# Optimization experiments

Measured on AMD Instinct MI355X. Metric: run time of the kernel, lower is better.

Reference implementation:

```python
import jax, jax.numpy as jnp
import numpy as np

N_POWER_SERIES = 8  # 'fixed' estimator, n_power_series=8, n_samples=4 (leading axis of v)


def _g_fn(x, W1, b1, W2, b2):
    # residual branch g(x): Linear -> ELU -> Linear (canonical i-ResNet block)
    return jax.nn.elu(x @ W1 + b1) @ W2 + b2


def setup_inputs() -> dict:
    key = jax.random.key(0)
    ks = jax.random.split(key, 4)
    B, D, H, S = 8192, 1024, 4096, 4
    x = jax.random.normal(ks[0], (B, D), jnp.float32)
    # scale weights so g is roughly contractive (Lipschitz < 1), as spectral norm enforces
    W1 = jax.random.normal(ks[1], (D, H), jnp.float32) * (0.5 / np.sqrt(D))
    b1 = jnp.zeros((H,), jnp.float32)
    W2 = jax.random.normal(ks[2], (H, D), jnp.float32) * (0.5 / np.sqrt(H))
    b2 = jnp.zeros((D,), jnp.float32)
    v = jax.random.normal(ks[3], (S, B, D), jnp.float32)  # Hutchinson probes
    log_df_dz = jnp.zeros((B,), jnp.float32)
    return {"x": x, "log_df_dz": log_df_dz, "W1": W1, "b1": b1, "W2": W2, "b2": b2, "v": v}


def reference(x, log_df_dz, W1, b1, W2, b2, v):
    g, vjp_fn = jax.vjp(lambda xx: _g_fn(xx, W1, b1, W2, b2), x)
    vjp = lambda w: vjp_fn(w)[0]  # w^T J, w: [B, D]

    w = v                      # [S, B, D]
    sum_diag = jnp.zeros(v.shape[:2], v.dtype)  # [S, B]
    for k in range(1, N_POWER_SERIES + 1):
        w = jax.vmap(vjp)(w)                        # v^T J^k
        inner = jnp.einsum('sbd,sbd->sb', w, v)     # Hutchinson tr(J^k) estimate
        sign = 1.0 if (k % 2 == 1) else -1.0
        sum_diag = sum_diag + sign * (inner / k)
    logdet = jnp.mean(sum_diag, axis=0)             # mean over samples -> [B]

    z = x + g
    return z, log_df_dz + logdet
```

## Files before the change

### kernel.cpp

```cpp
#include <hip/hip_runtime.h>
#include <hip/hip_bf16.h>

using bf16 = __hip_bfloat16;
typedef __attribute__((ext_vector_type(8))) short bf16x8;
typedef __attribute__((ext_vector_type(4))) float f32x4;

__device__ __forceinline__ float b2f(unsigned short u) {
  union { unsigned int i; float f; } x; x.i = ((unsigned int)u) << 16; return x.f;
}
__device__ __forceinline__ unsigned short f2b(float f) {
  __hip_bfloat16 h = __float2bfloat16(f);
  return *reinterpret_cast<unsigned short*>(&h);
}

__device__ __forceinline__ void load16_to_lds(const bf16* g, void* lds) {
  __builtin_amdgcn_global_load_lds((const __attribute__((address_space(1))) void*)g,
                                   (__attribute__((address_space(3))) void*)lds, 16, 0, 0);
}

#define FENCE() asm volatile("" ::: "memory")
#define BAR() do { FENCE(); __builtin_amdgcn_s_barrier(); FENCE(); } while (0)
#define SCHED_PIN() __builtin_amdgcn_sched_barrier(0)

__global__ void cast_f32_bf16(const float* __restrict__ in, bf16* __restrict__ out, size_t n) {
  size_t i0 = ((size_t)blockIdx.x * 256 + threadIdx.x) * 4;
  size_t stride = (size_t)gridDim.x * 256 * 4;
  for (size_t i = i0; i < n; i += stride) {
    float4 f = *(const float4*)(in + i);
    ushort4 o;
    o.x = f2b(f.x); o.y = f2b(f.y); o.z = f2b(f.z); o.w = f2b(f.w);
    *(ushort4*)(out + i) = o;
  }
}

__global__ void transpose_cast(const float* __restrict__ in, bf16* __restrict__ out, int R, int C) {
  __shared__ float tile[32][33];
  int tx = threadIdx.x & 31, ty = threadIdx.x >> 5;
  int r0 = blockIdx.y * 32, c0 = blockIdx.x * 32;
  #pragma unroll
  for (int i = 0; i < 32; i += 8)
    tile[ty + i][tx] = in[(size_t)(r0 + ty + i) * C + (c0 + tx)];
  __syncthreads();
  #pragma unroll
  for (int i = 0; i < 32; i += 8)
    out[(size_t)(c0 + ty + i) * R + (r0 + tx)] = __float2bfloat16(tile[tx][ty + i]);
}

template<int EPI>
__global__ __launch_bounds__(512, 2)
void gemm256(const bf16* __restrict__ A, const bf16* __restrict__ Bm,
             int M, int N, int K,
             bf16* __restrict__ OutB,
             const float* __restrict__ bias,
             const bf16* __restrict__ Ea) {
  __shared__ __align__(16) char pool[131072];
  char* Albs = pool;
  char* Blbs = pool + 65536;
  const int tid = threadIdx.x;
  const int l = tid & 63, w = tid >> 6;
  const int lane16 = l & 15, lh = l >> 4;
  const int wr = w >> 2, wc = w & 3;
  const int bm0 = blockIdx.y * 256, bn0 = blockIdx.x * 256;
  const int NT2 = K >> 7;

  auto stage = [&](const bf16* G, int grow0, int kbase, char* ldsbase) {
    #pragma unroll
    for (int r = 0; r < 2; ++r) {
      int p = (r * 512 + tid) * 16;
      int row = p >> 7, colb = p & 127;
      int cs = colb ^ ((row & 7) << 4);
      const bf16* g = G + (size_t)(grow0 + row) * K + kbase + (cs >> 1);
      load16_to_lds(g, ldsbase + (size_t)(r * 512 + w * 64) * 16);
    }
  };
  auto rd = [&](const char* base, int row, int colb) -> bf16x8 {
    return *(const bf16x8*)(base + row * 128 + (colb ^ ((row & 7) << 4)));
  };

  f32x4 acc[8][4] = {};
  bf16x8 a_r[4][2], b_r[4][2];

  #define RD_A(mq, buf) { _Pragma("unroll") for (int i = 0; i < 4; ++i) \
      _Pragma("unroll") for (int kk = 0; kk < 2; ++kk) \
      a_r[i][kk] = rd(Albs + (buf) * 32768, wr * 128 + (mq) * 64 + i * 16 + lane16, kk * 64 + lh * 16); }
  #define RD_B(buf) { _Pragma("unroll") for (int nf = 0; nf < 4; ++nf) \
      _Pragma("unroll") for (int kk = 0; kk < 2; ++kk) \
      b_r[nf][kk] = rd(Blbs + (buf) * 32768, wc * 64 + nf * 16 + lane16, kk * 64 + lh * 16); }
  #define MFMA_H(mq, n0) { __builtin_amdgcn_s_setprio(1); \
      _Pragma("unroll") for (int i = 0; i < 4; ++i) \
      _Pragma("unroll") for (int nn = 0; nn < 2; ++nn) \
      _Pragma("unroll") for (int kk = 0; kk < 2; ++kk) \
        acc[(mq)*4+i][(n0)+nn] = __builtin_amdgcn_mfma_f32_16x16x32_bf16( \
            a_r[i][kk], b_r[(n0)+nn][kk], acc[(mq)*4+i][(n0)+nn], 0, 0, 0); \
      __builtin_amdgcn_s_setprio(0); }
  #define PHASE(BODY_PRE, MFMA_CALL) { BODY_PRE; BAR(); SCHED_PIN(); MFMA_CALL; SCHED_PIN(); BAR(); }

  stage(Bm, bn0 + 0,   0,  Blbs + 0);
  stage(Bm, bn0 + 128, 0,  Blbs + 16384);
  stage(A,  bm0 + 0,   0,  Albs + 0);
  stage(A,  bm0 + 128, 0,  Albs + 16384);
  stage(Bm, bn0 + 0,   64, Blbs + 32768);
  stage(Bm, bn0 + 128, 64, Blbs + 32768 + 16384);
  stage(A,  bm0 + 0,   64, Albs + 32768);
  asm volatile("s_waitcnt vmcnt(6)" ::: "memory");
  SCHED_PIN();
  BAR();

  for (int t = 0; t < NT2; ++t) {
    const int k2 = (2 * t + 2) * 64, k3 = (2 * t + 3) * 64;
    const bool nl = (t < NT2 - 1);
    PHASE({ RD_B(0); RD_A(0, 0); stage(A, bm0 + 128, (2 * t + 1) * 64, Albs + 32768 + 16384); },
          MFMA_H(0, 0));
    PHASE({ if (nl) stage(Bm, bn0 + 0, k2, Blbs + 0); }, MFMA_H(0, 2));
    PHASE({ RD_A(1, 0); if (nl) stage(Bm, bn0 + 128, k2, Blbs + 16384); }, MFMA_H(1, 0));
    { if (nl) stage(A, bm0 + 0, k2, Albs + 0);
      BAR(); SCHED_PIN(); MFMA_H(1, 2); SCHED_PIN();
      if (nl) { asm volatile("s_waitcnt vmcnt(6)" ::: "memory"); }
      else    { asm volatile("s_waitcnt vmcnt(0)" ::: "memory"); }
      SCHED_PIN(); BAR(); }
    PHASE({ RD_B(1); RD_A(0, 1); if (nl) stage(A, bm0 + 128, k2, Albs + 16384); },
          MFMA_H(0, 0));
    PHASE({ if (nl) stage(Bm, bn0 + 0, k3, Blbs + 32768); }, MFMA_H(0, 2));
    PHASE({ RD_A(1, 1); if (nl) stage(Bm, bn0 + 128, k3, Blbs + 32768 + 16384); }, MFMA_H(1, 0));
    { if (nl) stage(A, bm0 + 0, k3, Albs + 32768);
      BAR(); SCHED_PIN(); MFMA_H(1, 2); SCHED_PIN();
      if (nl) { asm volatile("s_waitcnt vmcnt(6)" ::: "memory"); }
      SCHED_PIN(); BAR(); }
  }

  float* scr = (float*)(pool + w * 4352);
  const int row0 = bm0 + wr * 128, col0 = bn0 + wc * 64;
  const int erow = l >> 3, ecol = (l & 7) * 8;
  f32x4 bias0 = {}, bias1 = {};
  bf16x8 ea_pre[8][2];
  if (EPI == 0) {
    bias0 = *(const f32x4*)&bias[col0 + ecol];
    bias1 = *(const f32x4*)&bias[col0 + ecol + 4];
  } else {
    #pragma unroll
    for (int mf = 0; mf < 8; ++mf)
      #pragma unroll
      for (int p = 0; p < 2; ++p) {
        int gm = row0 + mf * 16 + p * 8 + erow;
        ea_pre[mf][p] = *(const bf16x8*)&Ea[(size_t)gm * N + col0 + ecol];
      }
  }
  SCHED_PIN();
  #pragma unroll
  for (int mf = 0; mf < 8; ++mf) {
    #pragma unroll
    for (int nf = 0; nf < 4; ++nf)
      #pragma unroll
      for (int q = 0; q < 4; ++q)
        scr[(lh * 4 + q) * 68 + nf * 16 + lane16] = acc[mf][nf][q];
    #pragma unroll
    for (int p = 0; p < 2; ++p) {
      int row = p * 8 + erow;
      const float* sp = &scr[row * 68 + ecol];
      f32x4 lo = *(const f32x4*)sp;
      f32x4 hi = *(const f32x4*)(sp + 4);
      int gm = row0 + mf * 16 + row;
      size_t idx = (size_t)gm * N + col0 + ecol;
      bf16x8 ov;
      if (EPI == 0) {
        #pragma unroll
        for (int j = 0; j < 8; ++j) {
          float fj = (j < 4) ? lo[j] : hi[j - 4];
          float bj = (j < 4) ? bias0[j] : bias1[j - 4];
          float hv = fj + bj;
          float a = hv > 0.f ? hv : expm1f(hv);
          ov[j] = (short)f2b(a);
        }
      } else {
        bf16x8 ea = ea_pre[mf][p];
        #pragma unroll
        for (int j = 0; j < 8; ++j) {
          float fj = (j < 4) ? lo[j] : hi[j - 4];
          float a = b2f((unsigned short)ea[j]);
          float e = a > 0.f ? 1.f : a + 1.f;
          ov[j] = (short)f2b(fj * e);
        }
      }
      *(bf16x8*)(&OutB[idx]) = ov;
    }
  }
  #undef RD_A
  #undef RD_B
  #undef MFMA_H
  #undef PHASE
}

template<int EPI>
__global__ __launch_bounds__(256)
void gemm_bt(const bf16* __restrict__ A, const bf16* __restrict__ Bm,
             int M, int N, int K,
             bf16* __restrict__ OutB, float* __restrict__ OutF,
             const float* __restrict__ bias, const float* __restrict__ Xadd) {
  __shared__ __align__(16) char pool[4 * 4352];
  bf16* As = (bf16*)pool;
  bf16* Bs = (bf16*)(pool + 8192);
  const int tid = threadIdx.x;
  const int l = tid & 63, w = tid >> 6;
  const int wr = w >> 1, wc = w & 1;
  const int lane16 = l & 15, lh = l >> 4;
  const int bm0 = blockIdx.x * 128, bn0 = blockIdx.y * 128;

  f32x4 acc[4][4] = {};
  const int nk = K >> 5;
  for (int kt = 0; kt < nk; ++kt) {
    const size_t kbase = (size_t)kt * 32;
    #pragma unroll
    for (int i = 0; i < 2; ++i) {
      int c = i * 256 + w * 64 + l;
      int row = c >> 2;
      int cbs = ((((c & 3) << 4) ^ ((row & 6) << 3)) >> 1);
      const bf16* ga = A  + (size_t)(bm0 + row) * K + kbase + cbs;
      const bf16* gb = Bm + (size_t)(bn0 + row) * K + kbase + cbs;
      char* la = (char*)As + (size_t)(i * 256 + w * 64) * 16;
      char* lb = (char*)Bs + (size_t)(i * 256 + w * 64) * 16;
      load16_to_lds(ga, la);
      load16_to_lds(gb, lb);
    }
    __syncthreads();
    bf16x8 af[4], bfv[4];
    #pragma unroll
    for (int r = 0; r < 4; ++r) {
      int arow = wr * 64 + r * 16 + lane16;
      int aoff = (lh << 4) ^ ((arow & 6) << 3);
      af[r] = *(const bf16x8*)((const char*)As + arow * 64 + aoff);
    }
    #pragma unroll
    for (int c = 0; c < 4; ++c) {
      int brow = wc * 64 + c * 16 + lane16;
      int boff = (lh << 4) ^ ((brow & 6) << 3);
      bfv[c] = *(const bf16x8*)((const char*)Bs + brow * 64 + boff);
    }
    #pragma unroll
    for (int r = 0; r < 4; ++r)
      #pragma unroll
      for (int c = 0; c < 4; ++c)
        acc[r][c] = __builtin_amdgcn_mfma_f32_16x16x32_bf16(af[r], bfv[c], acc[r][c], 0, 0, 0);
    __syncthreads();
  }

  if (EPI == 1) {
    #pragma unroll
    for (int r = 0; r < 4; ++r) {
      int gm_base = bm0 + wr * 64 + r * 16 + lh * 4;
      #pragma unroll
      for (int c = 0; c < 4; ++c) {
        int gn = bn0 + wc * 64 + c * 16 + lane16;
        #pragma unroll
        for (int q = 0; q < 4; ++q) {
          size_t idx = (size_t)(gm_base + q) * N + gn;
          OutF[idx] = acc[r][c][q] + bias[gn] + Xadd[idx];
        }
      }
    }
  } else {
    float* scr = (float*)(pool + w * 4352);
    #pragma unroll
    for (int r = 0; r < 4; ++r) {
      #pragma unroll
      for (int c = 0; c < 4; ++c)
        #pragma unroll
        for (int q = 0; q < 4; ++q)
          scr[(lh * 4 + q) * 68 + c * 16 + lane16] = acc[r][c][q];
      #pragma unroll
      for (int p = 0; p < 2; ++p) {
        int row = p * 8 + (l >> 3);
        int c0 = (l & 7) * 8;
        const float* sp = &scr[row * 68 + c0];
        f32x4 lo = *(const f32x4*)sp;
        f32x4 hi = *(const f32x4*)(sp + 4);
        int gm = bm0 + wr * 64 + r * 16 + row;
        int gn = bn0 + wc * 64 + c0;
        size_t idx = (size_t)gm * N + gn;
        bf16x8 ov;
        #pragma unroll
        for (int j = 0; j < 8; ++j) {
          float fj = (j < 4) ? lo[j] : hi[j - 4];
          ov[j] = (short)f2b(fj);
        }
        *(bf16x8*)(&OutB[idx]) = ov;
      }
      __syncthreads();
    }
  }
}

__global__ void rowdot(const bf16* __restrict__ W, const float* __restrict__ V,
                       float* __restrict__ sumdiag, float coef, int D) {
  size_t row = blockIdx.x;
  const unsigned short* wr = (const unsigned short*)W + row * D;
  const float* vr = V + row * D;
  int t = threadIdx.x;
  float s = 0.f;
  for (int i = t * 4; i < D; i += 256 * 4) {
    ushort4 a = *(const ushort4*)(wr + i);
    float4  b = *(const float4*)(vr + i);
    s += b2f(a.x) * b.x + b2f(a.y) * b.y + b2f(a.z) * b.z + b2f(a.w) * b.w;
  }
  #pragma unroll
  for (int o = 32; o > 0; o >>= 1) s += __shfl_down(s, o);
  __shared__ float red[4];
  if ((t & 63) == 0) red[t >> 6] = s;
  __syncthreads();
  if (t == 0) sumdiag[row] += coef * (red[0] + red[1] + red[2] + red[3]);
}

__global__ void finalize(const float* __restrict__ ldz, const float* __restrict__ sd,
                         float* __restrict__ out, int B, int S) {
  int b = blockIdx.x * 256 + threadIdx.x;
  if (b >= B) return;
  float acc = 0.f;
  for (int s = 0; s < S; ++s) acc += sd[(size_t)s * B + b];
  out[b] = ldz[b] + acc / (float)S;
}

extern "C" void kernel_launch(void* const* d_in, const int* in_sizes, int n_in,
                              void* d_out, int out_size, void* d_ws, size_t ws_size,
                              hipStream_t stream) {
  const int B = 8192, D = 1024, H = 4096, S = 4, NPS = 8;
  const float* x   = (const float*)d_in[0];
  const float* ldz = (const float*)d_in[1];
  const float* W1  = (const float*)d_in[2];
  const float* b1  = (const float*)d_in[3];
  const float* W2  = (const float*)d_in[4];
  const float* b2  = (const float*)d_in[5];
  const float* v   = (const float*)d_in[6];
  float* z_out  = (float*)d_out;
  float* ld_out = z_out + (size_t)B * D;

  char* ws = (char*)d_ws;
  size_t off = 0;
  auto alloc = [&](size_t bytes) {
    char* p = ws + off; off = (off + bytes + 255) & ~(size_t)255; return p;
  };
  float* sumdiag = (float*)alloc((size_t)S * B * 4);
  bf16* W1b  = (bf16*)alloc((size_t)D * H * 2);
  bf16* W2b  = (bf16*)alloc((size_t)D * H * 2);
  bf16* W1T  = (bf16*)alloc((size_t)D * H * 2);
  bf16* W2T  = (bf16*)alloc((size_t)D * H * 2);
  bf16* xb   = (bf16*)alloc((size_t)B * D * 2);
  bf16* abuf = (bf16*)alloc((size_t)B * H * 2);
  bf16* tbuf = (bf16*)alloc((size_t)B * H * 2);
  (void)ws_size; (void)in_sizes; (void)n_in; (void)out_size;

  hipMemsetAsync(sumdiag, 0, (size_t)S * B * 4, stream);

  cast_f32_bf16<<<1024, 256, 0, stream>>>(x,  xb,  (size_t)B * D);
  cast_f32_bf16<<<1024, 256, 0, stream>>>(W1, W1b, (size_t)D * H);
  cast_f32_bf16<<<1024, 256, 0, stream>>>(W2, W2b, (size_t)D * H);
  transpose_cast<<<dim3(H / 32, D / 32), 256, 0, stream>>>(W1, W1T, D, H);
  transpose_cast<<<dim3(D / 32, H / 32), 256, 0, stream>>>(W2, W2T, H, D);

  gemm256<0><<<dim3(H / 256, B / 256), 512, 0, stream>>>(xb, W1T, B, H, D,
      abuf, b1, nullptr);
  gemm_bt<1><<<dim3(B / 128, D / 128), 256, 0, stream>>>(abuf, W2T, B, D, H,
      nullptr, z_out, b2, x);

  bf16* wcur = xb;
  for (int s = 0; s < S; ++s) {
    const float* vs = v + (size_t)s * B * D;
    cast_f32_bf16<<<1024, 256, 0, stream>>>(vs, wcur, (size_t)B * D);
    for (int k = 1; k <= NPS; ++k) {
      gemm256<2><<<dim3(H / 256, B / 256), 512, 0, stream>>>(wcur, W2b, B, H, D,
          tbuf, nullptr, abuf);
      gemm_bt<3><<<dim3(B / 128, D / 128), 256, 0, stream>>>(tbuf, W1b, B, D, H,
          wcur, nullptr, nullptr, nullptr);
      float coef = ((k & 1) ? 1.f : -1.f) / (float)k;
      rowdot<<<B, 256, 0, stream>>>(wcur, vs, sumdiag + (size_t)s * B, coef, D);
    }
  }
  finalize<<<B / 256, 256, 0, stream>>>(ldz, sumdiag, ld_out, B, S);
}
```

Measured before the change: 6.126 ms.

## Batch two Hutchinson samples per GEMM launch when workspace allows

When the workspace is large enough, two probe samples are stacked along M and pushed through each power-series GEMM pair and rowdot in one launch, which halves the launch count and doubles the grid size. The ELU-derivative epilogue wraps the row index with a mask so both stacked samples read the same activation rows. Buffers are re-laid out so xb, W1T and W2T alias the temporary region. The cost is a larger workspace footprint, and the fixed mask ties the kernel to B=8192.

Result: slower. 6.422 ms (+4.8%).

```diff
diff --git a/kernel.cpp b/kernel.cpp
--- a/kernel.cpp
+++ b/kernel.cpp
@@ -142,7 +142,7 @@
       #pragma unroll
       for (int p = 0; p < 2; ++p) {
         int gm = row0 + mf * 16 + p * 8 + erow;
-        ea_pre[mf][p] = *(const bf16x8*)&Ea[(size_t)gm * N + col0 + ecol];
+        ea_pre[mf][p] = *(const bf16x8*)&Ea[(size_t)(gm & 8191) * N + col0 + ecol];
       }
   }
   SCHED_PIN();
@@ -332,6 +332,8 @@
   float* z_out  = (float*)d_out;
   float* ld_out = z_out + (size_t)B * D;
 
+  const int NS = (ws_size >= (size_t)252 * 1024 * 1024) ? 2 : 1;
+
   char* ws = (char*)d_ws;
   size_t off = 0;
   auto alloc = [&](size_t bytes) {
@@ -340,12 +342,13 @@
   float* sumdiag = (float*)alloc((size_t)S * B * 4);
   bf16* W1b  = (bf16*)alloc((size_t)D * H * 2);
   bf16* W2b  = (bf16*)alloc((size_t)D * H * 2);
-  bf16* W1T  = (bf16*)alloc((size_t)D * H * 2);
-  bf16* W2T  = (bf16*)alloc((size_t)D * H * 2);
-  bf16* xb   = (bf16*)alloc((size_t)B * D * 2);
   bf16* abuf = (bf16*)alloc((size_t)B * H * 2);
-  bf16* tbuf = (bf16*)alloc((size_t)B * H * 2);
-  (void)ws_size; (void)in_sizes; (void)n_in; (void)out_size;
+  bf16* wreg = (bf16*)alloc((size_t)NS * B * D * 2);
+  bf16* treg = (bf16*)alloc((size_t)NS * B * H * 2);
+  bf16* xb  = treg;
+  bf16* W1T = (bf16*)((char*)treg + (size_t)16 * 1024 * 1024);
+  bf16* W2T = (bf16*)((char*)treg + (size_t)24 * 1024 * 1024);
+  (void)in_sizes; (void)n_in; (void)out_size;
 
   hipMemsetAsync(sumdiag, 0, (size_t)S * B * 4, stream);
 
@@ -360,17 +363,17 @@
   gemm_bt<1><<<dim3(B / 128, D / 128), 256, 0, stream>>>(abuf, W2T, B, D, H,
       nullptr, z_out, b2, x);
 
-  bf16* wcur = xb;
-  for (int s = 0; s < S; ++s) {
-    const float* vs = v + (size_t)s * B * D;
-    cast_f32_bf16<<<1024, 256, 0, stream>>>(vs, wcur, (size_t)B * D);
+  for (int s0 = 0; s0 < S; s0 += NS) {
+    const float* vs = v + (size_t)s0 * B * D;
+    const int Mcur = NS * B;
+    cast_f32_bf16<<<2048, 256, 0, stream>>>(vs, wreg, (size_t)Mcur * D);
     for (int k = 1; k <= NPS; ++k) {
-      gemm256<2><<<dim3(H / 256, B / 256), 512, 0, stream>>>(wcur, W2b, B, H, D,
-          tbuf, nullptr, abuf);
-      gemm_bt<3><<<dim3(B / 128, D / 128), 256, 0, stream>>>(tbuf, W1b, B, D, H,
-          wcur, nullptr, nullptr, nullptr);
+      gemm256<2><<<dim3(H / 256, Mcur / 256), 512, 0, stream>>>(wreg, W2b, Mcur, H, D,
+          treg, nullptr, abuf);
+      gemm_bt<3><<<dim3(Mcur / 128, D / 128), 256, 0, stream>>>(treg, W1b, Mcur, D, H,
+          wreg, nullptr, nullptr, nullptr);
       float coef = ((k & 1) ? 1.f : -1.f) / (float)k;
-      rowdot<<<B, 256, 0, stream>>>(wcur, vs, sumdiag + (size_t)s * B, coef, D);
+      rowdot<<<Mcur, 256, 0, stream>>>(wreg, vs, sumdiag + (size_t)s0 * B, coef, D);
     }
   }
   finalize<<<B / 256, 256, 0, stream>>>(ldz, sumdiag, ld_out, B, S);
```
